# Kernel tuning notes

Hardware: AMD Instinct MI355X
Metric: run time of the kernel (lower is better)

The kernel has to match this reference:

```python
import jax, jax.numpy as jnp
import numpy as np

NEG_INF_FILL = -1000000.0  # matches torch code's masked fill value


def setup_inputs() -> dict:
    key = jax.random.key(0)
    kK, kV, kQ, kL = jax.random.split(key, 4)
    B, Sq, Sk, d, dv = 8, 2048, 2048, 512, 512
    return {
        "K": jax.random.normal(kK, (B, Sk, d), dtype=jnp.float32),
        "V": jax.random.normal(kV, (B, Sk, dv), dtype=jnp.float32),
        "Q": jax.random.normal(kQ, (B, Sq, d), dtype=jnp.float32),
        "valid_len": jax.random.randint(kL, (Sq,), 0, dv, dtype=jnp.int64),
    }


def reference(K, V, Q, valid_len):
    d = K.shape[-1]
    # score: [B, Sq, Sk]
    score = jnp.einsum("bqd,bkd->bqk", Q, K) / jnp.sqrt(jnp.asarray(d, Q.dtype))
    # x: [B, Sq, dv] -- NOTE: original applies mask+softmax to score @ V
    x = jnp.einsum("bqk,bkv->bqv", score, V)
    dv = x.shape[-1]
    # mask rows: per-query-position valid_len compared to feature index 0..dv-1
    mask = jnp.arange(dv)[None, :] > valid_len[:, None]  # [Sq, dv]
    x = jnp.where(mask[None, :, :], jnp.asarray(NEG_INF_FILL, x.dtype), x)
    return jax.nn.softmax(x, axis=-1)
```

## Files before the change

kernel.cpp:

```cpp
#include <hip/hip_runtime.h>
#include <hip/hip_bf16.h>
#include <math.h>

#define BATCH 8
#define SQ 2048
#define SK 2048
#define DD 512
#define DV 512
#define RP 40

typedef short bf16x8_t __attribute__((ext_vector_type(8)));
typedef float f32x4_t __attribute__((ext_vector_type(4)));

__device__ __forceinline__ unsigned int pk_bf16(float a, float b) {
    __hip_bfloat162 h = __float22bfloat162_rn(float2{a, b});
    unsigned int u;
    __builtin_memcpy(&u, &h, 4);
    return u;
}
__device__ __forceinline__ float from_hi(unsigned int u) {
    return __builtin_bit_cast(float, u);
}

__global__ __launch_bounds__(256) void ktv_mfma(const float* __restrict__ Kp,
                                                const float* __restrict__ Vp,
                                                float* __restrict__ Mpart) {
    const int b  = blockIdx.z & 7;
    const int ts = blockIdx.z >> 3;
    const int d0 = blockIdx.x * 128;
    const int v0 = blockIdx.y * 128;
    const float* Kb = Kp + (size_t)b * SK * DD;
    const float* Vb = Vp + (size_t)b * SK * DV;

    __shared__ __align__(16) unsigned short Kh[128 * RP], Kl[128 * RP],
                                            Vh[128 * RP], Vl[128 * RP];

    const int tid  = threadIdx.x;
    const int lane = tid & 63;
    const int w    = tid >> 6;
    const int wd   = (w & 1) * 64;
    const int wv   = (w >> 1) * 64;
    const int uu   = tid >> 5;
    const int xx   = tid & 31;

    f32x4_t acc[4][4];
#pragma unroll
    for (int i = 0; i < 4; ++i)
#pragma unroll
        for (int j = 0; j < 4; ++j) acc[i][j] = (f32x4_t){0.f, 0.f, 0.f, 0.f};

    const int tb = ts * 512;
    for (int t0 = 0; t0 < 512; t0 += 32) {
#pragma unroll
        for (int p = 0; p < 2; ++p) {
            const int t  = 16 * p + 2 * uu;
            const int to = (t >> 3) * 8 + (t & 7);
            const size_t gr = (size_t)(tb + t0 + t);
#pragma unroll
            for (int c = 0; c < 4; ++c) {
                const int d   = xx + 32 * c;
                const int off = d * RP + to;
                {
                    const float f0 = Kb[gr * DD + d0 + d];
                    const float f1 = Kb[(gr + 1) * DD + d0 + d];
                    const unsigned int h = pk_bf16(f0, f1);
                    const float r0 = f0 - from_hi(h << 16);
                    const float r1 = f1 - from_hi(h & 0xFFFF0000u);
                    *(unsigned int*)(Kh + off) = h;
                    *(unsigned int*)(Kl + off) = pk_bf16(r0, r1);
                }
                {
                    const float f0 = Vb[gr * DV + v0 + d];
                    const float f1 = Vb[(gr + 1) * DV + v0 + d];
                    const unsigned int h = pk_bf16(f0, f1);
                    const float r0 = f0 - from_hi(h << 16);
                    const float r1 = f1 - from_hi(h & 0xFFFF0000u);
                    *(unsigned int*)(Vh + off) = h;
                    *(unsigned int*)(Vl + off) = pk_bf16(r0, r1);
                }
            }
        }
        __syncthreads();

        const int kq = lane >> 4;
        const int mr = lane & 15;
        bf16x8_t ah[4], al_[4];
#pragma unroll
        for (int tm = 0; tm < 4; ++tm) {
            const int off = (wd + tm * 16 + mr) * RP + kq * 8;
            ah[tm]  = *(const bf16x8_t*)(Kh + off);
            al_[tm] = *(const bf16x8_t*)(Kl + off);
        }
#pragma unroll
        for (int tn = 0; tn < 4; ++tn) {
            const int off = (wv + tn * 16 + mr) * RP + kq * 8;
            const bf16x8_t bh = *(const bf16x8_t*)(Vh + off);
            const bf16x8_t bl = *(const bf16x8_t*)(Vl + off);
#pragma unroll
            for (int tm = 0; tm < 4; ++tm) {
                acc[tm][tn] = __builtin_amdgcn_mfma_f32_16x16x32_bf16(ah[tm], bh, acc[tm][tn], 0, 0, 0);
                acc[tm][tn] = __builtin_amdgcn_mfma_f32_16x16x32_bf16(ah[tm], bl, acc[tm][tn], 0, 0, 0);
                acc[tm][tn] = __builtin_amdgcn_mfma_f32_16x16x32_bf16(al_[tm], bh, acc[tm][tn], 0, 0, 0);
            }
        }
        __syncthreads();
    }

    float* Mp = Mpart + (size_t)(ts * 8 + b) * DD * DV;
    const int quad = lane >> 4;
    const int col  = lane & 15;
#pragma unroll
    for (int tm = 0; tm < 4; ++tm)
#pragma unroll
        for (int tn = 0; tn < 4; ++tn)
#pragma unroll
            for (int r = 0; r < 4; ++r) {
                const int d = d0 + wd + tm * 16 + quad * 4 + r;
                const int v = v0 + wv + tn * 16 + col;
                Mp[(size_t)d * DV + v] = acc[tm][tn][r];
            }
}

__global__ __launch_bounds__(256) void reduce_cvt(const float* __restrict__ Mpart,
                                                  unsigned short* __restrict__ Mth,
                                                  unsigned short* __restrict__ Mtl) {
    const int b  = blockIdx.z;
    const int d0 = blockIdx.x * 64;
    const int v0 = blockIdx.y * 64;
    __shared__ float T[64][65];
    const int i  = threadIdx.x;
    const int xr = i >> 4;
    const int xc = i & 15;

#pragma unroll
    for (int e = 0; e < 4; ++e) {
        const int dr = e * 16 + xr;
        float sx = 0.f, sy = 0.f, sz = 0.f, sw = 0.f;
#pragma unroll
        for (int sl = 0; sl < 4; ++sl) {
            const float4 f = *(const float4*)&Mpart[((size_t)(sl * 8 + b) * DD + d0 + dr) * DV + v0 + xc * 4];
            sx += f.x; sy += f.y; sz += f.z; sw += f.w;
        }
        T[dr][xc * 4 + 0] = sx;
        T[dr][xc * 4 + 1] = sy;
        T[dr][xc * 4 + 2] = sz;
        T[dr][xc * 4 + 3] = sw;
    }
    __syncthreads();

    const float s = 0.04419417382415922f;
#pragma unroll
    for (int e = 0; e < 4; ++e) {
        const int v = e * 16 + xr;
        float m[4], r[4];
        unsigned int hv[2], lv[2];
#pragma unroll
        for (int j = 0; j < 4; ++j) m[j] = T[xc * 4 + j][v] * s;
#pragma unroll
        for (int j = 0; j < 2; ++j) {
            hv[j] = pk_bf16(m[2 * j], m[2 * j + 1]);
            r[2 * j]     = m[2 * j]     - from_hi(hv[j] << 16);
            r[2 * j + 1] = m[2 * j + 1] - from_hi(hv[j] & 0xFFFF0000u);
            lv[j] = pk_bf16(r[2 * j], r[2 * j + 1]);
        }
        const size_t o = ((size_t)b * DV + v0 + v) * DD + d0 + xc * 4;
        *(uint2*)&Mth[o] = make_uint2(hv[0], hv[1]);
        *(uint2*)&Mtl[o] = make_uint2(lv[0], lv[1]);
    }
}

__global__ __launch_bounds__(256) void qm_mfma(const float* __restrict__ Qp,
                                               const unsigned short* __restrict__ Mth,
                                               const unsigned short* __restrict__ Mtl,
                                               float* __restrict__ Xp) {
    const int b  = blockIdx.z;
    const int q0 = blockIdx.x * 128;
    const int v0 = blockIdx.y * 128;
    const float* Qb = Qp + (size_t)b * SQ * DD;
    const unsigned short* Bhg = Mth + (size_t)b * DV * DD;
    const unsigned short* Blg = Mtl + (size_t)b * DV * DD;

    __shared__ __align__(16) unsigned short Qh[128 * RP], Ql[128 * RP],
                                            Bh[128 * RP], Bl[128 * RP];

    const int tid  = threadIdx.x;
    const int lane = tid & 63;
    const int w    = tid >> 6;
    const int wq   = (w & 1) * 64;
    const int wv   = (w >> 1) * 64;

    f32x4_t acc[4][4];
#pragma unroll
    for (int i = 0; i < 4; ++i)
#pragma unroll
        for (int j = 0; j < 4; ++j) acc[i][j] = (f32x4_t){0.f, 0.f, 0.f, 0.f};

    for (int k0 = 0; k0 < DD; k0 += 32) {
#pragma unroll
        for (int p = 0; p < 4; ++p) {
            const int q  = p * 32 + (tid >> 3);
            const int dc = (tid & 7) * 4;
            const float4 f = *(const float4*)&Qb[(size_t)(q0 + q) * DD + k0 + dc];
            const unsigned int h01 = pk_bf16(f.x, f.y);
            const unsigned int h23 = pk_bf16(f.z, f.w);
            const float r0 = f.x - from_hi(h01 << 16);
            const float r1 = f.y - from_hi(h01 & 0xFFFF0000u);
            const float r2 = f.z - from_hi(h23 << 16);
            const float r3 = f.w - from_hi(h23 & 0xFFFF0000u);
            const int off = q * RP + dc;
            *(uint2*)(Qh + off) = make_uint2(h01, h23);
            *(uint2*)(Ql + off) = make_uint2(pk_bf16(r0, r1), pk_bf16(r2, r3));
        }
#pragma unroll
        for (int p = 0; p < 2; ++p) {
            const int v  = p * 64 + (tid >> 2);
            const int kq = tid & 3;
            const int off = v * RP + kq * 8;
            *(bf16x8_t*)(Bh + off) = *(const bf16x8_t*)&Bhg[(size_t)(v0 + v) * DD + k0 + kq * 8];
            *(bf16x8_t*)(Bl + off) = *(const bf16x8_t*)&Blg[(size_t)(v0 + v) * DD + k0 + kq * 8];
        }
        __syncthreads();

        const int kq = lane >> 4;
        const int mr = lane & 15;
        bf16x8_t ah[4], al_[4];
#pragma unroll
        for (int tm = 0; tm < 4; ++tm) {
            const int off = (wq + tm * 16 + mr) * RP + kq * 8;
            ah[tm]  = *(const bf16x8_t*)(Qh + off);
            al_[tm] = *(const bf16x8_t*)(Ql + off);
        }
#pragma unroll
        for (int tn = 0; tn < 4; ++tn) {
            const int off = (wv + tn * 16 + mr) * RP + kq * 8;
            const bf16x8_t bh = *(const bf16x8_t*)(Bh + off);
            const bf16x8_t bl = *(const bf16x8_t*)(Bl + off);
#pragma unroll
            for (int tm = 0; tm < 4; ++tm) {
                acc[tm][tn] = __builtin_amdgcn_mfma_f32_16x16x32_bf16(ah[tm], bh, acc[tm][tn], 0, 0, 0);
                acc[tm][tn] = __builtin_amdgcn_mfma_f32_16x16x32_bf16(ah[tm], bl, acc[tm][tn], 0, 0, 0);
                acc[tm][tn] = __builtin_amdgcn_mfma_f32_16x16x32_bf16(al_[tm], bh, acc[tm][tn], 0, 0, 0);
            }
        }
        __syncthreads();
    }

    float* Xb = Xp + (size_t)b * SQ * DV;
    const int quad = lane >> 4;
    const int col  = lane & 15;
#pragma unroll
    for (int tm = 0; tm < 4; ++tm)
#pragma unroll
        for (int tn = 0; tn < 4; ++tn)
#pragma unroll
            for (int r = 0; r < 4; ++r)
                Xb[(size_t)(q0 + wq + tm * 16 + quad * 4 + r) * DV + v0 + wv + tn * 16 + col] = acc[tm][tn][r];
}

__global__ __launch_bounds__(256) void softmax_kernel(float* __restrict__ X,
                                                      const int* __restrict__ vlen) {
    const int wave = threadIdx.x >> 6;
    const int lane = threadIdx.x & 63;
    const int row  = blockIdx.x * 4 + wave;
    const int q    = row & (SQ - 1);
    float* xr = X + (size_t)row * DV;
    const int vl = vlen[q];

    float v[8];
#pragma unroll
    for (int u = 0; u < 2; ++u) {
        const int j0 = u * 256 + lane * 4;
        const float4 f = *(const float4*)&xr[j0];
        v[u * 4 + 0] = (j0 + 0 > vl) ? -1.0e6f : f.x;
        v[u * 4 + 1] = (j0 + 1 > vl) ? -1.0e6f : f.y;
        v[u * 4 + 2] = (j0 + 2 > vl) ? -1.0e6f : f.z;
        v[u * 4 + 3] = (j0 + 3 > vl) ? -1.0e6f : f.w;
    }

    float m = v[0];
#pragma unroll
    for (int i = 1; i < 8; ++i) m = fmaxf(m, v[i]);
#pragma unroll
    for (int off = 32; off > 0; off >>= 1) m = fmaxf(m, __shfl_xor(m, off, 64));

    float s = 0.f;
#pragma unroll
    for (int i = 0; i < 8; ++i) {
        v[i] = __expf(v[i] - m);
        s += v[i];
    }
#pragma unroll
    for (int off = 32; off > 0; off >>= 1) s += __shfl_xor(s, off, 64);

    const float inv = 1.0f / s;
#pragma unroll
    for (int u = 0; u < 2; ++u) {
        const int j0 = u * 256 + lane * 4;
        float4 o;
        o.x = v[u * 4 + 0] * inv;
        o.y = v[u * 4 + 1] * inv;
        o.z = v[u * 4 + 2] * inv;
        o.w = v[u * 4 + 3] * inv;
        *(float4*)&xr[j0] = o;
    }
}

extern "C" void kernel_launch(void* const* d_in, const int* in_sizes, int n_in,
                              void* d_out, int out_size, void* d_ws, size_t ws_size,
                              hipStream_t stream) {
    const float* Kp   = (const float*)d_in[0];
    const float* Vp   = (const float*)d_in[1];
    const float* Qp   = (const float*)d_in[2];
    const int*   vlen = (const int*)d_in[3];
    float* out = (float*)d_out;

    unsigned short* Mth = (unsigned short*)d_ws;
    unsigned short* Mtl = Mth + (size_t)BATCH * DD * DV;
    float* Mpart = out;

    ktv_mfma<<<dim3(4, 4, 32), 256, 0, stream>>>(Kp, Vp, Mpart);
    reduce_cvt<<<dim3(8, 8, 8), 256, 0, stream>>>(Mpart, Mth, Mtl);
    qm_mfma<<<dim3(16, 4, 8), 256, 0, stream>>>(Qp, Mth, Mtl, out);
    softmax_kernel<<<dim3(BATCH * SQ / 4), 256, 0, stream>>>(out, vlen);
}
```

Baseline: 208.6 us.

## Replace split-K reduce kernel with atomic accumulation and fuse bf16 split into QM load

The K^T V kernel now splits the sequence into 8 chunks instead of 4 and accumulates partial products straight into a zeroed fp32 workspace with atomicAdd, which removes the separate reduce/convert kernel. The Q·M kernel reads fp32 M directly, applies the scale, and does the bf16 hi/lo split while staging into shared memory, using 64-wide V tiles to double the grid. This saves one launch and the partial-sum round trip. In exchange it adds a memset, atomic traffic, redundant per-block conversion of M, and non-deterministic summation order.

```diff
diff --git a/kernel.cpp b/kernel.cpp
--- a/kernel.cpp
+++ b/kernel.cpp
@@ -24,7 +24,7 @@
 
 __global__ __launch_bounds__(256) void ktv_mfma(const float* __restrict__ Kp,
                                                 const float* __restrict__ Vp,
-                                                float* __restrict__ Mpart) {
+                                                float* __restrict__ Mg) {
     const int b  = blockIdx.z & 7;
     const int ts = blockIdx.z >> 3;
     const int d0 = blockIdx.x * 128;
@@ -49,8 +49,8 @@
 #pragma unroll
         for (int j = 0; j < 4; ++j) acc[i][j] = (f32x4_t){0.f, 0.f, 0.f, 0.f};
 
-    const int tb = ts * 512;
-    for (int t0 = 0; t0 < 512; t0 += 32) {
+    const int tb = ts * 256;
+    for (int t0 = 0; t0 < 256; t0 += 32) {
 #pragma unroll
         for (int p = 0; p < 2; ++p) {
             const int t  = 16 * p + 2 * uu;
@@ -106,7 +106,7 @@
         __syncthreads();
     }
 
-    float* Mp = Mpart + (size_t)(ts * 8 + b) * DD * DV;
+    float* Mb = Mg + (size_t)b * DD * DV;
     const int quad = lane >> 4;
     const int col  = lane & 15;
 #pragma unroll
@@ -117,83 +117,35 @@
             for (int r = 0; r < 4; ++r) {
                 const int d = d0 + wd + tm * 16 + quad * 4 + r;
                 const int v = v0 + wv + tn * 16 + col;
-                Mp[(size_t)d * DV + v] = acc[tm][tn][r];
-            }
-}
-
-__global__ __launch_bounds__(256) void reduce_cvt(const float* __restrict__ Mpart,
-                                                  unsigned short* __restrict__ Mth,
-                                                  unsigned short* __restrict__ Mtl) {
-    const int b  = blockIdx.z;
-    const int d0 = blockIdx.x * 64;
-    const int v0 = blockIdx.y * 64;
-    __shared__ float T[64][65];
-    const int i  = threadIdx.x;
-    const int xr = i >> 4;
-    const int xc = i & 15;
-
-#pragma unroll
-    for (int e = 0; e < 4; ++e) {
-        const int dr = e * 16 + xr;
-        float sx = 0.f, sy = 0.f, sz = 0.f, sw = 0.f;
-#pragma unroll
-        for (int sl = 0; sl < 4; ++sl) {
-            const float4 f = *(const float4*)&Mpart[((size_t)(sl * 8 + b) * DD + d0 + dr) * DV + v0 + xc * 4];
-            sx += f.x; sy += f.y; sz += f.z; sw += f.w;
-        }
-        T[dr][xc * 4 + 0] = sx;
-        T[dr][xc * 4 + 1] = sy;
-        T[dr][xc * 4 + 2] = sz;
-        T[dr][xc * 4 + 3] = sw;
-    }
-    __syncthreads();
-
-    const float s = 0.04419417382415922f;
-#pragma unroll
-    for (int e = 0; e < 4; ++e) {
-        const int v = e * 16 + xr;
-        float m[4], r[4];
-        unsigned int hv[2], lv[2];
-#pragma unroll
-        for (int j = 0; j < 4; ++j) m[j] = T[xc * 4 + j][v] * s;
-#pragma unroll
-        for (int j = 0; j < 2; ++j) {
-            hv[j] = pk_bf16(m[2 * j], m[2 * j + 1]);
-            r[2 * j]     = m[2 * j]     - from_hi(hv[j] << 16);
-            r[2 * j + 1] = m[2 * j + 1] - from_hi(hv[j] & 0xFFFF0000u);
-            lv[j] = pk_bf16(r[2 * j], r[2 * j + 1]);
-        }
-        const size_t o = ((size_t)b * DV + v0 + v) * DD + d0 + xc * 4;
-        *(uint2*)&Mth[o] = make_uint2(hv[0], hv[1]);
-        *(uint2*)&Mtl[o] = make_uint2(lv[0], lv[1]);
-    }
+                atomicAdd(&Mb[(size_t)d * DV + v], acc[tm][tn][r]);
+            }
 }
 
 __global__ __launch_bounds__(256) void qm_mfma(const float* __restrict__ Qp,
-                                               const unsigned short* __restrict__ Mth,
-                                               const unsigned short* __restrict__ Mtl,
+                                               const float* __restrict__ Mg,
                                                float* __restrict__ Xp) {
     const int b  = blockIdx.z;
     const int q0 = blockIdx.x * 128;
-    const int v0 = blockIdx.y * 128;
+    const int v0 = blockIdx.y * 64;
     const float* Qb = Qp + (size_t)b * SQ * DD;
-    const unsigned short* Bhg = Mth + (size_t)b * DV * DD;
-    const unsigned short* Blg = Mtl + (size_t)b * DV * DD;
+    const float* Mb = Mg + (size_t)b * DD * DV;
 
     __shared__ __align__(16) unsigned short Qh[128 * RP], Ql[128 * RP],
-                                            Bh[128 * RP], Bl[128 * RP];
+                                            Bh[64 * RP], Bl[64 * RP];
 
     const int tid  = threadIdx.x;
     const int lane = tid & 63;
     const int w    = tid >> 6;
     const int wq   = (w & 1) * 64;
-    const int wv   = (w >> 1) * 64;
-
-    f32x4_t acc[4][4];
+    const int wv   = (w >> 1) * 32;
+
+    f32x4_t acc[4][2];
 #pragma unroll
     for (int i = 0; i < 4; ++i)
 #pragma unroll
-        for (int j = 0; j < 4; ++j) acc[i][j] = (f32x4_t){0.f, 0.f, 0.f, 0.f};
+        for (int j = 0; j < 2; ++j) acc[i][j] = (f32x4_t){0.f, 0.f, 0.f, 0.f};
+
+    const float s = 0.04419417382415922f;
 
     for (int k0 = 0; k0 < DD; k0 += 32) {
 #pragma unroll
@@ -211,13 +163,22 @@
             *(uint2*)(Qh + off) = make_uint2(h01, h23);
             *(uint2*)(Ql + off) = make_uint2(pk_bf16(r0, r1), pk_bf16(r2, r3));
         }
-#pragma unroll
-        for (int p = 0; p < 2; ++p) {
-            const int v  = p * 64 + (tid >> 2);
-            const int kq = tid & 3;
-            const int off = v * RP + kq * 8;
-            *(bf16x8_t*)(Bh + off) = *(const bf16x8_t*)&Bhg[(size_t)(v0 + v) * DD + k0 + kq * 8];
-            *(bf16x8_t*)(Bl + off) = *(const bf16x8_t*)&Blg[(size_t)(v0 + v) * DD + k0 + kq * 8];
+        {
+            const int kp = tid >> 4;
+            const int k  = 2 * kp;
+            const int vx = tid & 15;
+#pragma unroll
+            for (int c = 0; c < 4; ++c) {
+                const int v = vx + 16 * c;
+                const float f0 = Mb[(size_t)(k0 + k) * DV + v0 + v] * s;
+                const float f1 = Mb[(size_t)(k0 + k + 1) * DV + v0 + v] * s;
+                const unsigned int h = pk_bf16(f0, f1);
+                const float r0 = f0 - from_hi(h << 16);
+                const float r1 = f1 - from_hi(h & 0xFFFF0000u);
+                const int off = v * RP + k;
+                *(unsigned int*)(Bh + off) = h;
+                *(unsigned int*)(Bl + off) = pk_bf16(r0, r1);
+            }
         }
         __syncthreads();
 
@@ -231,7 +192,7 @@
             al_[tm] = *(const bf16x8_t*)(Ql + off);
         }
 #pragma unroll
-        for (int tn = 0; tn < 4; ++tn) {
+        for (int tn = 0; tn < 2; ++tn) {
             const int off = (wv + tn * 16 + mr) * RP + kq * 8;
             const bf16x8_t bh = *(const bf16x8_t*)(Bh + off);
             const bf16x8_t bl = *(const bf16x8_t*)(Bl + off);
@@ -251,7 +212,7 @@
 #pragma unroll
     for (int tm = 0; tm < 4; ++tm)
 #pragma unroll
-        for (int tn = 0; tn < 4; ++tn)
+        for (int tn = 0; tn < 2; ++tn)
 #pragma unroll
             for (int r = 0; r < 4; ++r)
                 Xb[(size_t)(q0 + wq + tm * 16 + quad * 4 + r) * DV + v0 + wv + tn * 16 + col] = acc[tm][tn][r];
@@ -283,16 +244,16 @@
 #pragma unroll
     for (int off = 32; off > 0; off >>= 1) m = fmaxf(m, __shfl_xor(m, off, 64));
 
-    float s = 0.f;
+    float ssum = 0.f;
 #pragma unroll
     for (int i = 0; i < 8; ++i) {
         v[i] = __expf(v[i] - m);
-        s += v[i];
-    }
-#pragma unroll
-    for (int off = 32; off > 0; off >>= 1) s += __shfl_xor(s, off, 64);
-
-    const float inv = 1.0f / s;
+        ssum += v[i];
+    }
+#pragma unroll
+    for (int off = 32; off > 0; off >>= 1) ssum += __shfl_xor(ssum, off, 64);
+
+    const float inv = 1.0f / ssum;
 #pragma unroll
     for (int u = 0; u < 2; ++u) {
         const int j0 = u * 256 + lane * 4;
@@ -313,13 +274,10 @@
     const float* Qp   = (const float*)d_in[2];
     const int*   vlen = (const int*)d_in[3];
     float* out = (float*)d_out;
-
-    unsigned short* Mth = (unsigned short*)d_ws;
-    unsigned short* Mtl = Mth + (size_t)BATCH * DD * DV;
-    float* Mpart = out;
-
-    ktv_mfma<<<dim3(4, 4, 32), 256, 0, stream>>>(Kp, Vp, Mpart);
-    reduce_cvt<<<dim3(8, 8, 8), 256, 0, stream>>>(Mpart, Mth, Mtl);
-    qm_mfma<<<dim3(16, 4, 8), 256, 0, stream>>>(Qp, Mth, Mtl, out);
+    float* M   = (float*)d_ws;
+
+    hipMemsetAsync(d_ws, 0, (size_t)BATCH * DD * DV * sizeof(float), stream);
+    ktv_mfma<<<dim3(4, 4, 64), 256, 0, stream>>>(Kp, Vp, M);
+    qm_mfma<<<dim3(16, 8, 8), 256, 0, stream>>>(Qp, M, out);
     softmax_kernel<<<dim3(BATCH * SQ / 4), 256, 0, stream>>>(out, vlen);
 }
```

Measured after the change: 257.7 us. 1.23x slower.
